# Optimization experiments

Measured on AMD Instinct MI355X. Metric: run time of the kernel, lower is better.

The kernel has to match this reference:

```python
import jax, jax.numpy as jnp
import numpy as np

S = 4096      # packed sequence length
DIM = 1024    # model dim
H = 8         # num heads
HD = 64       # per-branch head dim (head_dim // 2 in the module)
LAMBDA_INIT = 0.8 - 0.6 * float(np.exp(-0.3 * 0.0))  # depth=0 -> 0.2
EPS = 1e-5


def setup_inputs() -> dict:
    key = jax.random.key(0)
    ks = jax.random.split(key, 10)
    P = 2 * H * HD  # = 1024
    return {
        "x": jax.random.normal(ks[0], (S, DIM), jnp.float32),
        "mask": jnp.ones((1, 1, S, S), jnp.bool_),
        "Wq": jax.random.normal(ks[1], (DIM, P), jnp.float32) * 0.02,
        "Wk": jax.random.normal(ks[2], (DIM, P), jnp.float32) * 0.02,
        "Wv": jax.random.normal(ks[3], (DIM, P), jnp.float32) * 0.02,
        "Wo": jax.random.normal(ks[4], (P, DIM), jnp.float32) * 0.02,
        "lambda_q1": jax.random.normal(ks[5], (HD,), jnp.float32) * 0.1,
        "lambda_k1": jax.random.normal(ks[6], (HD,), jnp.float32) * 0.1,
        "lambda_q2": jax.random.normal(ks[7], (HD,), jnp.float32) * 0.1,
        "lambda_k2": jax.random.normal(ks[8], (HD,), jnp.float32) * 0.1,
        "subln_weight": jnp.ones((2 * HD,), jnp.float32),
    }


def reference(x, mask, Wq, Wk, Wv, Wo, lambda_q1, lambda_k1, lambda_q2,
              lambda_k2, subln_weight):
    # projections: (S, 2H, HD) split into branch index along a new axis
    xq = (x @ Wq).reshape(S, H, 2, HD)   # [2*H] view -> (H,2) contiguous split
    xk = (x @ Wk).reshape(S, H, 2, HD)
    xv = (x @ Wv).reshape(S, H, 2 * HD)
    q1, q2 = xq[:, :, 0], xq[:, :, 1]    # (S,H,HD)
    k1, k2 = xk[:, :, 0], xk[:, :, 1]

    scale = 1.0 / jnp.sqrt(jnp.float32(HD))
    bias = jnp.where(mask[0, 0], 0.0, -jnp.inf)  # (S,S) additive mask

    def sdpa(q, k):
        # q,k: (S,H,HD); xv: (S,H,2HD)
        scores = jnp.einsum('shd,thd->hst', q, k) * scale + bias  # (H,S,S)
        p = jax.nn.softmax(scores, axis=-1)
        return jnp.einsum('hst,thd->shd', p, xv)                  # (S,H,2HD)

    attn1 = sdpa(q1, k1)
    attn2 = sdpa(q2, k2)

    lam1 = jnp.exp(jnp.sum(lambda_q1 * lambda_k1))
    lam2 = jnp.exp(jnp.sum(lambda_q2 * lambda_k2))
    lambda_full = lam1 - lam2 + LAMBDA_INIT

    attn = attn1 - lambda_full * attn2                            # (S,H,2HD)
    # RMSNorm over last dim (2*HD) with learnable weight
    attn = attn * jax.lax.rsqrt(jnp.mean(attn * attn, axis=-1, keepdims=True) + EPS)
    attn = attn * subln_weight
    attn = attn * (1.0 - LAMBDA_INIT)
    return attn.reshape(S, H * 2 * HD) @ Wo                       # (S, DIM)
```

## Files before the change

### kernel.cpp

```cpp
#include <hip/hip_runtime.h>
#include <hip/hip_bf16.h>
#include <type_traits>
#include <utility>


using bf16 = __hip_bfloat16;

static constexpr int SQ = 4096;
static constexpr int DM = 1024;
static constexpr float LAMB_INIT = 0.2f;
static constexpr float KSC = 0.18033688011112043f;

typedef float  f32x4    __attribute__((ext_vector_type(4)));
typedef short  s16x4    __attribute__((ext_vector_type(4)));
typedef short  bf16x8_i __attribute__((ext_vector_type(8)));
typedef __bf16 bf16x8_b __attribute__((ext_vector_type(8)));

template<typename T, typename = void> struct mfma_ok : std::false_type {};
template<typename T> struct mfma_ok<T, std::void_t<decltype(
    __builtin_amdgcn_mfma_f32_16x16x32_bf16(std::declval<T>(), std::declval<T>(),
                                            std::declval<f32x4>(), 0, 0, 0))>>
    : std::true_type {};
using abfrag = std::conditional_t<mfma_ok<bf16x8_b>::value, bf16x8_b, bf16x8_i>;

__device__ __forceinline__ f32x4 mfma16(abfrag a, abfrag b, f32x4 c) {
    return __builtin_amdgcn_mfma_f32_16x16x32_bf16(a, b, c, 0, 0, 0);
}
__device__ __forceinline__ abfrag ldfrag(const bf16* p) {
    return *reinterpret_cast<const abfrag*>(p);
}
__device__ __forceinline__ short bf2s(bf16 b) {
    short s; __builtin_memcpy(&s, &b, 2); return s;
}
__device__ __forceinline__ float fexp2(float x) {
#if __has_builtin(__builtin_amdgcn_exp2f)
    return __builtin_amdgcn_exp2f(x);
#else
    return exp2f(x);
#endif
}
__device__ __forceinline__ int cvtpk(float lo, float hi) {
    int r;
    asm("v_cvt_pk_bf16_f32 %0, %1, %2" : "=v"(r) : "v"(lo), "v"(hi));
    return r;
}
__device__ __forceinline__ void gld_lds16(const bf16* g, bf16* l) {
    __builtin_amdgcn_global_load_lds((__attribute__((address_space(1))) void*)g,
                                     (__attribute__((address_space(3))) void*)l,
                                     16, 0, 0);
}


__global__ __launch_bounds__(256) void convert_x(const float* __restrict__ in,
                                                 bf16* __restrict__ outp)
{
    const size_t i = ((size_t)blockIdx.x * 256 + threadIdx.x) * 4;
    const f32x4 v = *reinterpret_cast<const f32x4*>(in + i);
    s16x4 o;
#pragma unroll
    for (int j = 0; j < 4; ++j) o[j] = bf2s(__float2bfloat16(v[j]));
    *reinterpret_cast<s16x4*>(outp + i) = o;
}

__global__ __launch_bounds__(256) void transpose_w(
    const float* __restrict__ Wq, const float* __restrict__ Wk,
    const float* __restrict__ Wv, const float* __restrict__ Wo,
    bf16* __restrict__ Wqt, bf16* __restrict__ Wkt,
    bf16* __restrict__ Wvt, bf16* __restrict__ Wot)
{
    const int z = blockIdx.z;
    const float* src = (z == 0) ? Wq : (z == 1) ? Wk : (z == 2) ? Wv : Wo;
    bf16* dst        = (z == 0) ? Wqt : (z == 1) ? Wkt : (z == 2) ? Wvt : Wot;
    const float scale = (z == 0) ? KSC : 1.0f;
    __shared__ float tbuf[32][33];
    const int k0 = blockIdx.x * 32, n0 = blockIdx.y * 32;
    const int c = threadIdx.x & 31, r0 = threadIdx.x >> 5;
#pragma unroll
    for (int i = 0; i < 4; ++i)
        tbuf[r0 + i * 8][c] = src[(size_t)(k0 + r0 + i * 8) * 1024 + n0 + c];
    __syncthreads();
#pragma unroll
    for (int i = 0; i < 4; ++i)
        dst[(size_t)(n0 + r0 + i * 8) * 1024 + k0 + c] =
            __float2bfloat16(tbuf[c][r0 + i * 8] * scale);
}

__global__ __launch_bounds__(256) void transpose_v(const bf16* __restrict__ V,
                                                   bf16* __restrict__ Vt)
{
    __shared__ bf16 tbuf[32][33];
    const int s0 = blockIdx.x * 32, n0 = blockIdx.y * 32;
    const int c = threadIdx.x & 31, r0 = threadIdx.x >> 5;
#pragma unroll
    for (int i = 0; i < 4; ++i)
        tbuf[r0 + i * 8][c] = V[(size_t)(s0 + r0 + i * 8) * 1024 + n0 + c];
    __syncthreads();
#pragma unroll
    for (int i = 0; i < 4; ++i)
        Vt[(size_t)(n0 + r0 + i * 8) * 4096 + s0 + c] = tbuf[c][r0 + i * 8];
}

__global__ void lambda_kernel(const float* lq1, const float* lk1,
                              const float* lq2, const float* lk2, float* outp)
{
    const int lane = threadIdx.x;
    float a = lq1[lane] * lk1[lane];
    float b = lq2[lane] * lk2[lane];
#pragma unroll
    for (int m = 1; m < 64; m <<= 1) {
        a += __shfl_xor(a, m, 64);
        b += __shfl_xor(b, m, 64);
    }
    if (lane == 0) outp[0] = __expf(a) - __expf(b) + LAMB_INIT;
}


template<bool BF16OUT>
__device__ __forceinline__ void gemm_core(const bf16* __restrict__ A,
                                          const bf16* __restrict__ Bt,
                                          void* __restrict__ Cout,
                                          int m0, int n0, int ldc)
{
    __shared__ __align__(16) bf16 As[128 * 32];
    __shared__ __align__(16) bf16 Bs[128 * 32];
    const int tid  = threadIdx.x;
    const int wid  = tid >> 6;
    const int lane = tid & 63;
    const int l15  = lane & 15;
    const int l4   = lane >> 4;
    const int wr   = wid >> 1;
    const int wc   = wid & 1;

    const f32x4 zero4 = {0.f, 0.f, 0.f, 0.f};
    f32x4 acc[4][4];
#pragma unroll
    for (int i = 0; i < 4; ++i)
#pragma unroll
        for (int j = 0; j < 4; ++j) acc[i][j] = zero4;

    for (int kt = 0; kt < 1024; kt += 32) {
        __syncthreads();
#pragma unroll
        for (int it = 0; it < 2; ++it) {
            const int flat = it * 256 + tid;
            const int row  = flat >> 2;
            const int c16  = flat & 3;
            const int ldst = (it * 256 + wid * 64) * 8;
            gld_lds16(&A [(size_t)(m0 + row) * 1024 + kt + c16 * 8], &As[ldst]);
            gld_lds16(&Bt[(size_t)(n0 + row) * 1024 + kt + c16 * 8], &Bs[ldst]);
        }
        __syncthreads();
        abfrag a[4], b[4];
#pragma unroll
        for (int mi = 0; mi < 4; ++mi)
            a[mi] = ldfrag(&As[(wr * 64 + mi * 16 + l15) * 32 + l4 * 8]);
#pragma unroll
        for (int ni = 0; ni < 4; ++ni)
            b[ni] = ldfrag(&Bs[(wc * 64 + ni * 16 + l15) * 32 + l4 * 8]);
#pragma unroll
        for (int mi = 0; mi < 4; ++mi)
#pragma unroll
            for (int ni = 0; ni < 4; ++ni)
                acc[mi][ni] = mfma16(a[mi], b[ni], acc[mi][ni]);
    }

#pragma unroll
    for (int mi = 0; mi < 4; ++mi)
#pragma unroll
        for (int ni = 0; ni < 4; ++ni)
#pragma unroll
            for (int r = 0; r < 4; ++r) {
                const int row = m0 + wr * 64 + mi * 16 + l4 * 4 + r;
                const int col = n0 + wc * 64 + ni * 16 + l15;
                if constexpr (BF16OUT)
                    ((bf16*)Cout)[(size_t)row * ldc + col] = __float2bfloat16(acc[mi][ni][r]);
                else
                    ((float*)Cout)[(size_t)row * ldc + col] = acc[mi][ni][r];
            }
}

__global__ __launch_bounds__(256, 3) void gemm_qkv(
    const bf16* __restrict__ xbf,
    const bf16* __restrict__ Wqt, const bf16* __restrict__ Wkt,
    const bf16* __restrict__ Wvt,
    bf16* __restrict__ Qo, bf16* __restrict__ Ko, bf16* __restrict__ Vo)
{
    const int which = blockIdx.y >> 3;
    const bf16* Bt = (which == 0) ? Wqt : (which == 1) ? Wkt : Wvt;
    bf16* Cp       = (which == 0) ? Qo  : (which == 1) ? Ko  : Vo;
    gemm_core<true>(xbf, Bt, Cp, blockIdx.x * 128, (blockIdx.y & 7) * 128, 1024);
}

__global__ __launch_bounds__(256, 3) void gemm_out(
    const bf16* __restrict__ Amat, const bf16* __restrict__ Wot,
    float* __restrict__ out)
{
    gemm_core<false>(Amat, Wot, out, blockIdx.x * 128, blockIdx.y * 128, 1024);
}


__global__ __launch_bounds__(512, 2) void flash_diff(
    const bf16* __restrict__ Qm, const bf16* __restrict__ Km,
    const bf16* __restrict__ Vtm, const float* __restrict__ lam_ptr,
    const float* __restrict__ subln, bf16* __restrict__ Amat)
{
    const int bid  = blockIdx.x;
    const int h    = bid & 7;
    const int qt   = bid >> 3;
    const int tid  = threadIdx.x;
    const int wid  = tid >> 6;
    const int lane = tid & 63;
    const int l15  = lane & 15;
    const int l4   = lane >> 4;
    const int qbase = qt * 128 + wid * 16;
    const int swz   = (l15 & 7) << 4;

    constexpr float THR = 8.0f;
    constexpr int KOFF = 0, VOFF = 49152, BUFSZ = 16384;

    __shared__ __align__(16) char smem[98304];

    abfrag qf[2][2];
#pragma unroll
    for (int c = 0; c < 2; ++c)
#pragma unroll
        for (int kc = 0; kc < 2; ++kc)
            qf[c][kc] = ldfrag(&Qm[(size_t)(qbase + l15) * DM +
                                   h * 128 + c * 64 + kc * 32 + l4 * 8]);
    asm volatile("" :: "v"(qf[0][0]), "v"(qf[0][1]), "v"(qf[1][0]), "v"(qf[1][1]));

    union { abfrag f; short s[8]; } uon;
#pragma unroll
    for (int i = 0; i < 8; ++i) uon.s[i] = (short)0x3F80;
    const abfrag ones = uon.f;

    const bf16* kap[2];
    const bf16* vap[2];
#pragma unroll
    for (int it = 0; it < 2; ++it) {
        const int slot = it * 512 + tid;
        const int krow = slot >> 4;
        const int kcb  = ((slot & 15) << 4) ^ ((krow & 7) << 4);
        kap[it] = Km + (size_t)krow * DM + h * 128 + (kcb >> 1);
        const int vrow = slot >> 3;
        const int vcb  = ((slot & 7) << 4) ^ ((vrow & 7) << 4);
        vap[it] = Vtm + (size_t)(h * 128 + vrow) * SQ + (vcb >> 1);
    }
    auto stage = [&](int buf) {
        char* kd = smem + KOFF + buf * BUFSZ;
        char* vd = smem + VOFF + buf * BUFSZ;
#pragma unroll
        for (int it = 0; it < 2; ++it) {
            gld_lds16(kap[it], (bf16*)(kd + (it * 512 + wid * 64) * 16));
            kap[it] += 64 * DM;
            gld_lds16(vap[it], (bf16*)(vd + (it * 512 + wid * 64) * 16));
            vap[it] += 64;
        }
    };

    const int kLane0 = l15 * 256 + ((l4 * 16) ^ swz);
    const int kLane1 = l15 * 256 + ((64 + l4 * 16) ^ swz);
    int vLane[4];
#pragma unroll
    for (int ch = 0; ch < 2; ++ch)
#pragma unroll
        for (int hh = 0; hh < 2; ++hh)
            vLane[ch * 2 + hh] = l15 * 128 + ((ch * 64 + hh * 32 + l4 * 8) ^ swz);

    const f32x4 zero4 = {0.f, 0.f, 0.f, 0.f};
    f32x4 o_[2][8];
#pragma unroll
    for (int c = 0; c < 2; ++c)
#pragma unroll
        for (int vt = 0; vt < 8; ++vt) o_[c][vt] = zero4;
    f32x4 lacc[2] = {zero4, zero4};
    float m_loc[2] = {0.f, 0.f};

    stage(0);
    stage(1);
    asm volatile("s_waitcnt vmcnt(4)" ::: "memory");
    __builtin_amdgcn_s_barrier();

    int cur = 0, nxt = 2;
    constexpr int NT = SQ / 64;
#pragma unroll 1
    for (int t = 0; t < NT; ++t) {
        const bool pf = (t + 2 < NT);
        if (pf) stage(nxt);

        const char* kbuf = smem + KOFF + cur * BUFSZ;
        const char* vbuf = smem + VOFF + cur * BUFSZ;
        const char* kb0  = kbuf + kLane0;
        const char* kb1  = kbuf + kLane1;

        abfrag pa[2][2];
#pragma unroll
        for (int c = 0; c < 2; ++c) {
            const float mc = m_loc[c];
            const f32x4 binit = {-mc, -mc, -mc, -mc};
            f32x4 sc[4];
#pragma unroll
            for (int j = 0; j < 4; ++j) {
                const abfrag k0 = *(const abfrag*)(kb0 + (j * 4096 + c * 128));
                const abfrag k1 = *(const abfrag*)(kb1 + (j * 4096 + c * 128));
                f32x4 z = mfma16(k0, qf[c][0], binit);
                sc[j] = mfma16(k1, qf[c][1], z);
            }
            float lmx = fmaxf(fmaxf(sc[0][0], sc[0][1]), fmaxf(sc[0][2], sc[0][3]));
#pragma unroll
            for (int j = 1; j < 4; ++j)
                lmx = fmaxf(lmx, fmaxf(fmaxf(sc[j][0], sc[j][1]),
                                       fmaxf(sc[j][2], sc[j][3])));
            if (__any(lmx > THR)) {
                float mx = lmx;
                mx = fmaxf(mx, __shfl_xor(mx, 16, 64));
                mx = fmaxf(mx, __shfl_xor(mx, 32, 64));
                const float alpha = fexp2(-mx);
                m_loc[c] += mx;
#pragma unroll
                for (int r = 0; r < 4; ++r) {
                    const float alr = __shfl(alpha, l4 * 4 + r, 64);
#pragma unroll
                    for (int vt = 0; vt < 8; ++vt) o_[c][vt][r] *= alr;
                    lacc[c][r] *= alr;
                }
#pragma unroll
                for (int j = 0; j < 4; ++j)
#pragma unroll
                    for (int r = 0; r < 4; ++r) sc[j][r] -= mx;
            }
            f32x4 pe[4];
#pragma unroll
            for (int j = 0; j < 4; ++j)
#pragma unroll
                for (int r = 0; r < 4; ++r) pe[j][r] = fexp2(sc[j][r]);
            union { abfrag f; int i[4]; } u0, u1;
            u0.i[0] = cvtpk(pe[0][0], pe[0][1]);
            u0.i[1] = cvtpk(pe[0][2], pe[0][3]);
            u0.i[2] = cvtpk(pe[1][0], pe[1][1]);
            u0.i[3] = cvtpk(pe[1][2], pe[1][3]);
            u1.i[0] = cvtpk(pe[2][0], pe[2][1]);
            u1.i[1] = cvtpk(pe[2][2], pe[2][3]);
            u1.i[2] = cvtpk(pe[3][0], pe[3][1]);
            u1.i[3] = cvtpk(pe[3][2], pe[3][3]);
            pa[c][0] = u0.f;
            pa[c][1] = u1.f;
        }

        const char* vb00 = vbuf + vLane[0];
        const char* vb01 = vbuf + vLane[1];
        const char* vb10 = vbuf + vLane[2];
        const char* vb11 = vbuf + vLane[3];

        __builtin_amdgcn_s_setprio(1);
        lacc[0] = mfma16(pa[0][0], ones, lacc[0]);
        lacc[0] = mfma16(pa[0][1], ones, lacc[0]);
        lacc[1] = mfma16(pa[1][0], ones, lacc[1]);
        lacc[1] = mfma16(pa[1][1], ones, lacc[1]);
#pragma unroll
        for (int vt = 0; vt < 8; ++vt) {
            union { abfrag f; s16x4 hh[2]; } v0, v1;
            v0.hh[0] = *(const s16x4*)(vb00 + vt * 2048);
            v0.hh[1] = *(const s16x4*)(vb01 + vt * 2048);
            v1.hh[0] = *(const s16x4*)(vb10 + vt * 2048);
            v1.hh[1] = *(const s16x4*)(vb11 + vt * 2048);
            o_[0][vt] = mfma16(pa[0][0], v0.f, o_[0][vt]);
            o_[1][vt] = mfma16(pa[1][0], v0.f, o_[1][vt]);
            o_[0][vt] = mfma16(pa[0][1], v1.f, o_[0][vt]);
            o_[1][vt] = mfma16(pa[1][1], v1.f, o_[1][vt]);
        }
        __builtin_amdgcn_s_setprio(0);

        if (pf) asm volatile("s_waitcnt vmcnt(4)" ::: "memory");
        else    asm volatile("s_waitcnt vmcnt(0)" ::: "memory");
        __builtin_amdgcn_s_barrier();
        cur = (cur == 2) ? 0 : cur + 1;
        nxt = (nxt == 2) ? 0 : nxt + 1;
    }

    const float lam = lam_ptr[0];
    float il1[4], il2[4];
#pragma unroll
    for (int r = 0; r < 4; ++r) {
        il1[r] = 1.f / lacc[0][r];
        il2[r] = lam / lacc[1][r];
    }
#pragma unroll
    for (int r = 0; r < 4; ++r) {
        float comb[8];
        float ss = 0.f;
#pragma unroll
        for (int vt = 0; vt < 8; ++vt) {
            const float v = o_[0][vt][r] * il1[r] - o_[1][vt][r] * il2[r];
            comb[vt] = v;
            ss += v * v;
        }
        ss += __shfl_xor(ss, 1, 64);
        ss += __shfl_xor(ss, 2, 64);
        ss += __shfl_xor(ss, 4, 64);
        ss += __shfl_xor(ss, 8, 64);
        const float rinv = rsqrtf(ss * (1.f / 128.f) + 1e-5f);
        const int row = qbase + l4 * 4 + r;
#pragma unroll
        for (int vt = 0; vt < 8; ++vt) {
            const float outv = comb[vt] * rinv * subln[vt * 16 + l15] * 0.8f;
            Amat[(size_t)row * DM + h * 128 + vt * 16 + l15] = __float2bfloat16(outv);
        }
    }
}


extern "C" void kernel_launch(void* const* d_in, const int* in_sizes, int n_in,
                              void* d_out, int out_size, void* d_ws, size_t ws_size,
                              hipStream_t stream)
{
    (void)in_sizes; (void)n_in; (void)out_size; (void)ws_size;
    const float* x    = (const float*)d_in[0];
    const float* Wq   = (const float*)d_in[2];
    const float* Wk   = (const float*)d_in[3];
    const float* Wv   = (const float*)d_in[4];
    const float* Wo   = (const float*)d_in[5];
    const float* lq1  = (const float*)d_in[6];
    const float* lk1  = (const float*)d_in[7];
    const float* lq2  = (const float*)d_in[8];
    const float* lk2  = (const float*)d_in[9];
    const float* subw = (const float*)d_in[10];

    char* ws = (char*)d_ws;
    size_t off = 0;
    auto take = [&](size_t n) { void* p = ws + off; off += (n + 255) & ~(size_t)255; return p; };
    bf16* xbf = (bf16*)take((size_t)SQ * DM * 2);
    bf16* Wqt = (bf16*)take((size_t)DM * DM * 2);
    bf16* Wkt = (bf16*)take((size_t)DM * DM * 2);
    bf16* Wvt = (bf16*)take((size_t)DM * DM * 2);
    bf16* Wot = (bf16*)take((size_t)DM * DM * 2);
    bf16* Qb  = (bf16*)take((size_t)SQ * DM * 2);
    bf16* Kb  = (bf16*)take((size_t)SQ * DM * 2);
    bf16* Vb  = (bf16*)take((size_t)SQ * DM * 2);
    bf16* Vtb = (bf16*)take((size_t)SQ * DM * 2);
    bf16* Am  = (bf16*)take((size_t)SQ * DM * 2);
    float* lamp = (float*)take(256);

    convert_x   <<<dim3(SQ * DM / 1024), dim3(256), 0, stream>>>(x, xbf);
    transpose_w <<<dim3(32, 32, 4),      dim3(256), 0, stream>>>(Wq, Wk, Wv, Wo, Wqt, Wkt, Wvt, Wot);
    lambda_kernel<<<dim3(1),             dim3(64),  0, stream>>>(lq1, lk1, lq2, lk2, lamp);
    gemm_qkv    <<<dim3(32, 24),         dim3(256), 0, stream>>>(xbf, Wqt, Wkt, Wvt, Qb, Kb, Vb);
    transpose_v <<<dim3(128, 32),        dim3(256), 0, stream>>>(Vb, Vtb);
    flash_diff  <<<dim3(256),            dim3(512), 0, stream>>>(Qb, Kb, Vtb, lamp, subw, Am);
    gemm_out    <<<dim3(32, 8),          dim3(256), 0, stream>>>(Am, Wot, (float*)d_out);
}
```

Measured before the change: 192.5 us.

## Double-buffer 128-key tiles and preload V fragments before score computation

Changes the flash-attention K/V staging from a 3-stage ring of 64-key tiles to a 2-stage ring of 128-key tiles, with two barriers per iteration and the wait placed before compute. Each 128-key tile is processed in two halves, and all V fragments for a half are loaded into registers before the QK^T and softmax work so the LDS reads overlap with it. The goal is fewer loop iterations and barriers per key, plus better hiding of LDS latency. In exchange, LDS use rises to 128 KB, which may cut occupancy below the two blocks per CU requested by launch_bounds, and holding the preloaded V fragments raises register pressure.

```diff
diff --git a/kernel.cpp b/kernel.cpp
--- a/kernel.cpp
+++ b/kernel.cpp
@@ -216,9 +216,9 @@
     const int swz   = (l15 & 7) << 4;
 
     constexpr float THR = 8.0f;
-    constexpr int KOFF = 0, VOFF = 49152, BUFSZ = 16384;
-
-    __shared__ __align__(16) char smem[98304];
+    constexpr int KOFF = 0, VOFF = 65536, BUFSZ = 32768;
+
+    __shared__ __align__(16) char smem[131072];
 
     abfrag qf[2][2];
 #pragma unroll
@@ -234,27 +234,25 @@
     for (int i = 0; i < 8; ++i) uon.s[i] = (short)0x3F80;
     const abfrag ones = uon.f;
 
-    const bf16* kap[2];
-    const bf16* vap[2];
-#pragma unroll
-    for (int it = 0; it < 2; ++it) {
-        const int slot = it * 512 + tid;
-        const int krow = slot >> 4;
-        const int kcb  = ((slot & 15) << 4) ^ ((krow & 7) << 4);
-        kap[it] = Km + (size_t)krow * DM + h * 128 + (kcb >> 1);
-        const int vrow = slot >> 3;
-        const int vcb  = ((slot & 7) << 4) ^ ((vrow & 7) << 4);
-        vap[it] = Vtm + (size_t)(h * 128 + vrow) * SQ + (vcb >> 1);
+    const bf16* kap[4];
+    const bf16* vap[4];
+#pragma unroll
+    for (int g = 0; g < 4; ++g) {
+        const int slot = g * 512 + tid;
+        const int row  = slot >> 4;
+        const int cb   = ((slot & 15) << 4) ^ ((row & 7) << 4);
+        kap[g] = Km + (size_t)row * DM + h * 128 + (cb >> 1);
+        vap[g] = Vtm + (size_t)(h * 128 + row) * SQ + (cb >> 1);
     }
     auto stage = [&](int buf) {
         char* kd = smem + KOFF + buf * BUFSZ;
         char* vd = smem + VOFF + buf * BUFSZ;
 #pragma unroll
-        for (int it = 0; it < 2; ++it) {
-            gld_lds16(kap[it], (bf16*)(kd + (it * 512 + wid * 64) * 16));
-            kap[it] += 64 * DM;
-            gld_lds16(vap[it], (bf16*)(vd + (it * 512 + wid * 64) * 16));
-            vap[it] += 64;
+        for (int g = 0; g < 4; ++g) {
+            gld_lds16(kap[g], (bf16*)(kd + (g * 512 + wid * 64) * 16));
+            kap[g] += 128 * DM;
+            gld_lds16(vap[g], (bf16*)(vd + (g * 512 + wid * 64) * 16));
+            vap[g] += 128;
         }
     };
 
@@ -265,7 +263,7 @@
     for (int ch = 0; ch < 2; ++ch)
 #pragma unroll
         for (int hh = 0; hh < 2; ++hh)
-            vLane[ch * 2 + hh] = l15 * 128 + ((ch * 64 + hh * 32 + l4 * 8) ^ swz);
+            vLane[ch * 2 + hh] = l15 * 256 + ((ch * 64 + hh * 32 + l4 * 8) ^ swz);
 
     const f32x4 zero4 = {0.f, 0.f, 0.f, 0.f};
     f32x4 o_[2][8];
@@ -277,105 +275,108 @@
     float m_loc[2] = {0.f, 0.f};
 
     stage(0);
-    stage(1);
-    asm volatile("s_waitcnt vmcnt(4)" ::: "memory");
-    __builtin_amdgcn_s_barrier();
-
-    int cur = 0, nxt = 2;
-    constexpr int NT = SQ / 64;
+
+    int cur = 0;
+    constexpr int NT = SQ / 128;
 #pragma unroll 1
     for (int t = 0; t < NT; ++t) {
-        const bool pf = (t + 2 < NT);
-        if (pf) stage(nxt);
+        const bool pf = (t + 1 < NT);
+        if (pf) stage(cur ^ 1);
+        if (pf) asm volatile("s_waitcnt vmcnt(8)" ::: "memory");
+        else    asm volatile("s_waitcnt vmcnt(0)" ::: "memory");
+        __builtin_amdgcn_s_barrier();
 
         const char* kbuf = smem + KOFF + cur * BUFSZ;
         const char* vbuf = smem + VOFF + cur * BUFSZ;
-        const char* kb0  = kbuf + kLane0;
-        const char* kb1  = kbuf + kLane1;
-
-        abfrag pa[2][2];
-#pragma unroll
-        for (int c = 0; c < 2; ++c) {
-            const float mc = m_loc[c];
-            const f32x4 binit = {-mc, -mc, -mc, -mc};
-            f32x4 sc[4];
-#pragma unroll
-            for (int j = 0; j < 4; ++j) {
-                const abfrag k0 = *(const abfrag*)(kb0 + (j * 4096 + c * 128));
-                const abfrag k1 = *(const abfrag*)(kb1 + (j * 4096 + c * 128));
-                f32x4 z = mfma16(k0, qf[c][0], binit);
-                sc[j] = mfma16(k1, qf[c][1], z);
+
+#pragma unroll
+        for (int h2 = 0; h2 < 2; ++h2) {
+            const char* kh = kbuf + h2 * 16384;
+            const char* vh = vbuf + h2 * 128;
+
+            union { abfrag f; s16x4 hh[2]; } vv0[8], vv1[8];
+#pragma unroll
+            for (int vt = 0; vt < 8; ++vt) {
+                vv0[vt].hh[0] = *(const s16x4*)(vh + vt * 4096 + vLane[0]);
+                vv0[vt].hh[1] = *(const s16x4*)(vh + vt * 4096 + vLane[1]);
+                vv1[vt].hh[0] = *(const s16x4*)(vh + vt * 4096 + vLane[2]);
+                vv1[vt].hh[1] = *(const s16x4*)(vh + vt * 4096 + vLane[3]);
             }
-            float lmx = fmaxf(fmaxf(sc[0][0], sc[0][1]), fmaxf(sc[0][2], sc[0][3]));
-#pragma unroll
-            for (int j = 1; j < 4; ++j)
-                lmx = fmaxf(lmx, fmaxf(fmaxf(sc[j][0], sc[j][1]),
-                                       fmaxf(sc[j][2], sc[j][3])));
-            if (__any(lmx > THR)) {
-                float mx = lmx;
-                mx = fmaxf(mx, __shfl_xor(mx, 16, 64));
-                mx = fmaxf(mx, __shfl_xor(mx, 32, 64));
-                const float alpha = fexp2(-mx);
-                m_loc[c] += mx;
-#pragma unroll
-                for (int r = 0; r < 4; ++r) {
-                    const float alr = __shfl(alpha, l4 * 4 + r, 64);
-#pragma unroll
-                    for (int vt = 0; vt < 8; ++vt) o_[c][vt][r] *= alr;
-                    lacc[c][r] *= alr;
+
+            const char* kb0 = kh + kLane0;
+            const char* kb1 = kh + kLane1;
+
+            abfrag pa[2][2];
+#pragma unroll
+            for (int c = 0; c < 2; ++c) {
+                const float mc = m_loc[c];
+                const f32x4 binit = {-mc, -mc, -mc, -mc};
+                f32x4 sc[4];
+#pragma unroll
+                for (int jj = 0; jj < 4; ++jj) {
+                    const abfrag k0 = *(const abfrag*)(kb0 + (jj * 4096 + c * 128));
+                    const abfrag k1 = *(const abfrag*)(kb1 + (jj * 4096 + c * 128));
+                    f32x4 z = mfma16(k0, qf[c][0], binit);
+                    sc[jj] = mfma16(k1, qf[c][1], z);
                 }
-#pragma unroll
-                for (int j = 0; j < 4; ++j)
-#pragma unroll
-                    for (int r = 0; r < 4; ++r) sc[j][r] -= mx;
+                float lmx = fmaxf(fmaxf(sc[0][0], sc[0][1]), fmaxf(sc[0][2], sc[0][3]));
+#pragma unroll
+                for (int jj = 1; jj < 4; ++jj)
+                    lmx = fmaxf(lmx, fmaxf(fmaxf(sc[jj][0], sc[jj][1]),
+                                           fmaxf(sc[jj][2], sc[jj][3])));
+                if (__any(lmx > THR)) {
+                    float mx = lmx;
+                    mx = fmaxf(mx, __shfl_xor(mx, 16, 64));
+                    mx = fmaxf(mx, __shfl_xor(mx, 32, 64));
+                    const float alpha = fexp2(-mx);
+                    m_loc[c] += mx;
+#pragma unroll
+                    for (int r = 0; r < 4; ++r) {
+                        const float alr = __shfl(alpha, l4 * 4 + r, 64);
+#pragma unroll
+                        for (int vt = 0; vt < 8; ++vt) o_[c][vt][r] *= alr;
+                        lacc[c][r] *= alr;
+                    }
+#pragma unroll
+                    for (int jj = 0; jj < 4; ++jj)
+#pragma unroll
+                        for (int r = 0; r < 4; ++r) sc[jj][r] -= mx;
+                }
+                f32x4 pe[4];
+#pragma unroll
+                for (int jj = 0; jj < 4; ++jj)
+#pragma unroll
+                    for (int r = 0; r < 4; ++r) pe[jj][r] = fexp2(sc[jj][r]);
+                union { abfrag f; int i[4]; } u0, u1;
+                u0.i[0] = cvtpk(pe[0][0], pe[0][1]);
+                u0.i[1] = cvtpk(pe[0][2], pe[0][3]);
+                u0.i[2] = cvtpk(pe[1][0], pe[1][1]);
+                u0.i[3] = cvtpk(pe[1][2], pe[1][3]);
+                u1.i[0] = cvtpk(pe[2][0], pe[2][1]);
+                u1.i[1] = cvtpk(pe[2][2], pe[2][3]);
+                u1.i[2] = cvtpk(pe[3][0], pe[3][1]);
+                u1.i[3] = cvtpk(pe[3][2], pe[3][3]);
+                pa[c][0] = u0.f;
+                pa[c][1] = u1.f;
             }
-            f32x4 pe[4];
-#pragma unroll
-            for (int j = 0; j < 4; ++j)
-#pragma unroll
-                for (int r = 0; r < 4; ++r) pe[j][r] = fexp2(sc[j][r]);
-            union { abfrag f; int i[4]; } u0, u1;
-            u0.i[0] = cvtpk(pe[0][0], pe[0][1]);
-            u0.i[1] = cvtpk(pe[0][2], pe[0][3]);
-            u0.i[2] = cvtpk(pe[1][0], pe[1][1]);
-            u0.i[3] = cvtpk(pe[1][2], pe[1][3]);
-            u1.i[0] = cvtpk(pe[2][0], pe[2][1]);
-            u1.i[1] = cvtpk(pe[2][2], pe[2][3]);
-            u1.i[2] = cvtpk(pe[3][0], pe[3][1]);
-            u1.i[3] = cvtpk(pe[3][2], pe[3][3]);
-            pa[c][0] = u0.f;
-            pa[c][1] = u1.f;
+
+            __builtin_amdgcn_s_setprio(1);
+            lacc[0] = mfma16(pa[0][0], ones, lacc[0]);
+            lacc[0] = mfma16(pa[0][1], ones, lacc[0]);
+            lacc[1] = mfma16(pa[1][0], ones, lacc[1]);
+            lacc[1] = mfma16(pa[1][1], ones, lacc[1]);
+#pragma unroll
+            for (int vt = 0; vt < 8; ++vt) {
+                o_[0][vt] = mfma16(pa[0][0], vv0[vt].f, o_[0][vt]);
+                o_[1][vt] = mfma16(pa[1][0], vv0[vt].f, o_[1][vt]);
+                o_[0][vt] = mfma16(pa[0][1], vv1[vt].f, o_[0][vt]);
+                o_[1][vt] = mfma16(pa[1][1], vv1[vt].f, o_[1][vt]);
+            }
+            __builtin_amdgcn_s_setprio(0);
         }
 
-        const char* vb00 = vbuf + vLane[0];
-        const char* vb01 = vbuf + vLane[1];
-        const char* vb10 = vbuf + vLane[2];
-        const char* vb11 = vbuf + vLane[3];
-
-        __builtin_amdgcn_s_setprio(1);
-        lacc[0] = mfma16(pa[0][0], ones, lacc[0]);
-        lacc[0] = mfma16(pa[0][1], ones, lacc[0]);
-        lacc[1] = mfma16(pa[1][0], ones, lacc[1]);
-        lacc[1] = mfma16(pa[1][1], ones, lacc[1]);
-#pragma unroll
-        for (int vt = 0; vt < 8; ++vt) {
-            union { abfrag f; s16x4 hh[2]; } v0, v1;
-            v0.hh[0] = *(const s16x4*)(vb00 + vt * 2048);
-            v0.hh[1] = *(const s16x4*)(vb01 + vt * 2048);
-            v1.hh[0] = *(const s16x4*)(vb10 + vt * 2048);
-            v1.hh[1] = *(const s16x4*)(vb11 + vt * 2048);
-            o_[0][vt] = mfma16(pa[0][0], v0.f, o_[0][vt]);
-            o_[1][vt] = mfma16(pa[1][0], v0.f, o_[1][vt]);
-            o_[0][vt] = mfma16(pa[0][1], v1.f, o_[0][vt]);
-            o_[1][vt] = mfma16(pa[1][1], v1.f, o_[1][vt]);
-        }
-        __builtin_amdgcn_s_setprio(0);
-
-        if (pf) asm volatile("s_waitcnt vmcnt(4)" ::: "memory");
-        else    asm volatile("s_waitcnt vmcnt(0)" ::: "memory");
         __builtin_amdgcn_s_barrier();
-        cur = (cur == 2) ? 0 : cur + 1;
-        nxt = (nxt == 2) ? 0 : nxt + 1;
+        cur ^= 1;
     }
 
     const float lam = lam_ptr[0];
```

New measurement: 214.4 us. 11.4% more time.
